# Kernel optimization log

Measured on AMD Instinct MI355X. Metric: run time of the kernel, lower is better.

## Reference

```python
import jax, jax.numpy as jnp
import numpy as np

UNITS = 256

def setup_inputs() -> dict:
    key = jax.random.key(0)
    k1, k2, k3, k4 = jax.random.split(key, 4)
    B, T, F = 131072, 7, 60
    x = jax.random.normal(k1, (B, T, F), dtype=jnp.float32)
    W = jax.random.normal(k2, (F, 4 * UNITS), dtype=jnp.float32) * 0.05
    U = jax.random.normal(k3, (UNITS, 4 * UNITS), dtype=jnp.float32) * 0.05
    b = jax.random.normal(k4, (4 * UNITS,), dtype=jnp.float32) * 0.05
    return {"x": x, "W": W, "U": U, "b": b}

def reference(x, W, U, b):
    # Keras LSTM, return_sequences=False, return_state=True -> (last_h, h, c).
    # Gate order in the fused kernel: i, f, c(g), o. Inference path (no dropout).
    B = x.shape[0]
    h0 = jnp.zeros((B, UNITS), dtype=x.dtype)
    c0 = jnp.zeros((B, UNITS), dtype=x.dtype)

    def step(carry, xt):
        h, c = carry
        z = xt @ W + h @ U + b  # [B, 4*UNITS]
        zi, zf, zg, zo = jnp.split(z, 4, axis=-1)
        i = jax.nn.sigmoid(zi)
        f = jax.nn.sigmoid(zf)
        g = jnp.tanh(zg)
        o = jax.nn.sigmoid(zo)
        c_new = f * c + i * g
        h_new = o * jnp.tanh(c_new)
        return (h_new, c_new), None

    xs = jnp.transpose(x, (1, 0, 2))  # [T, B, F]
    (h, c), _ = jax.lax.scan(step, (h0, c0), xs)
    return h, h, c
```

## Files before the change

### kernel.cpp

```cpp
#include <hip/hip_runtime.h>

typedef __bf16 bf16x8 __attribute__((ext_vector_type(8)));
typedef float f32x4 __attribute__((ext_vector_type(4)));

#define TSTEPS 7
#define FEAT 60
#define MTILE 64
#define THREADS 256

__global__ void prep_U_kernel(const float* __restrict__ U, __bf16* __restrict__ Ut) {
    int idx = blockIdx.x * blockDim.x + threadIdx.x;
    int n = idx >> 8;
    int k = idx & 255;
    Ut[idx] = (__bf16)U[k * 1024 + n];
}

__global__ void prep_W_kernel(const float* __restrict__ W, __bf16* __restrict__ Wt) {
    int idx = blockIdx.x * blockDim.x + threadIdx.x;
    int n = idx >> 6;
    int k = idx & 63;
    float v = (k < FEAT) ? W[k * 1024 + n] : 0.0f;
    Wt[idx] = (__bf16)v;
}

__device__ __forceinline__ float sigm(float z) {
    return __builtin_amdgcn_rcpf(1.0f + __expf(-z));
}
__device__ __forceinline__ float tanh_(float z) {
    return 1.0f - 2.0f * __builtin_amdgcn_rcpf(__expf(2.0f * z) + 1.0f);
}

__global__ __launch_bounds__(THREADS, 2)
void lstm_kernel(const float* __restrict__ x, const __bf16* __restrict__ Ut,
                 const __bf16* __restrict__ Wt, const float* __restrict__ bias,
                 float* __restrict__ out, int B) {
    __shared__ __align__(16) __bf16 x_lds[2][MTILE][72];
    __shared__ __align__(16) __bf16 h_lds[MTILE][264];

    const int tid = threadIdx.x;
    const int wave = tid >> 6;
    const int lane = tid & 63;
    const int quad = lane >> 4;
    const int l16 = lane & 15;
    const int r0 = blockIdx.x * MTILE;

    for (int i = tid; i < 2 * MTILE * 4; i += THREADS) {
        int bb = i >> 8;
        int rem = i & 255;
        x_lds[bb][rem >> 2][FEAT + (rem & 3)] = (__bf16)0.0f;
    }

    auto stage_x = [&](int t, int b) {
        for (int i = tid; i < MTILE * 15; i += THREADS) {
            int m = i / 15;
            int q = i - m * 15;
            const float4 v =
                *(const float4*)&x[((size_t)(r0 + m) * TSTEPS + t) * FEAT + q * 4];
            __bf16* dst = &x_lds[b][m][q * 4];
            dst[0] = (__bf16)v.x;
            dst[1] = (__bf16)v.y;
            dst[2] = (__bf16)v.z;
            dst[3] = (__bf16)v.w;
        }
    };

    stage_x(0, 0);

    float c_reg[4][4][4];
#pragma unroll
    for (int uc = 0; uc < 4; ++uc)
#pragma unroll
        for (int mt = 0; mt < 4; ++mt)
#pragma unroll
            for (int r = 0; r < 4; ++r) c_reg[uc][mt][r] = 0.0f;

    float bvals[4][4];
#pragma unroll
    for (int uc = 0; uc < 4; ++uc)
#pragma unroll
        for (int g = 0; g < 4; ++g)
            bvals[uc][g] = bias[g * 256 + wave * 64 + uc * 16 + l16];

    __syncthreads();

    const size_t HN = (size_t)B * 256;

    for (int t = 0; t < TSTEPS; ++t) {
        const int xb = t & 1;
        bf16x8 a[4][10];
        if (t > 0) {
#pragma unroll
            for (int mt = 0; mt < 4; ++mt)
#pragma unroll
                for (int kf = 0; kf < 8; ++kf)
                    a[mt][kf] = *(const bf16x8*)&h_lds[mt * 16 + l16][kf * 32 + quad * 8];
        }
#pragma unroll
        for (int mt = 0; mt < 4; ++mt) {
            a[mt][8] = *(const bf16x8*)&x_lds[xb][mt * 16 + l16][quad * 8];
            a[mt][9] = *(const bf16x8*)&x_lds[xb][mt * 16 + l16][32 + quad * 8];
        }
        __syncthreads();

        if (t + 1 < TSTEPS) stage_x(t + 1, xb ^ 1);

#pragma unroll
        for (int uc = 0; uc < 4; ++uc) {
            const int ncol = wave * 64 + uc * 16 + l16;
            f32x4 acc[4];

            auto gate_gemm = [&](int g) {
                const __bf16* uRow = Ut + (size_t)(g * 256 + ncol) * 256;
                const __bf16* wRow = Wt + (size_t)(g * 256 + ncol) * 64;
                bf16x8 bfr[10];
                if (t > 0) {
#pragma unroll
                    for (int kf = 0; kf < 8; ++kf)
                        bfr[kf] = *(const bf16x8*)(uRow + kf * 32 + quad * 8);
                }
#pragma unroll
                for (int kf = 0; kf < 2; ++kf)
                    bfr[8 + kf] = *(const bf16x8*)(wRow + kf * 32 + quad * 8);
#pragma unroll
                for (int mt = 0; mt < 4; ++mt) acc[mt] = (f32x4){0.f, 0.f, 0.f, 0.f};
                if (t > 0) {
#pragma unroll
                    for (int kf = 0; kf < 8; ++kf)
#pragma unroll
                        for (int mt = 0; mt < 4; ++mt)
                            acc[mt] = __builtin_amdgcn_mfma_f32_16x16x32_bf16(
                                a[mt][kf], bfr[kf], acc[mt], 0, 0, 0);
                }
#pragma unroll
                for (int kf = 0; kf < 2; ++kf)
#pragma unroll
                    for (int mt = 0; mt < 4; ++mt)
                        acc[mt] = __builtin_amdgcn_mfma_f32_16x16x32_bf16(
                            a[mt][8 + kf], bfr[8 + kf], acc[mt], 0, 0, 0);
            };

            float iv[4][4], pg[4][4];
            gate_gemm(0);
#pragma unroll
            for (int mt = 0; mt < 4; ++mt)
#pragma unroll
                for (int r = 0; r < 4; ++r)
                    iv[mt][r] = sigm(acc[mt][r] + bvals[uc][0]);
            gate_gemm(2);
#pragma unroll
            for (int mt = 0; mt < 4; ++mt)
#pragma unroll
                for (int r = 0; r < 4; ++r)
                    pg[mt][r] = iv[mt][r] * tanh_(acc[mt][r] + bvals[uc][2]);
            gate_gemm(1);
#pragma unroll
            for (int mt = 0; mt < 4; ++mt)
#pragma unroll
                for (int r = 0; r < 4; ++r)
                    c_reg[uc][mt][r] =
                        sigm(acc[mt][r] + bvals[uc][1]) * c_reg[uc][mt][r] + pg[mt][r];
            gate_gemm(3);
#pragma unroll
            for (int mt = 0; mt < 4; ++mt)
#pragma unroll
                for (int r = 0; r < 4; ++r) {
                    float cc = c_reg[uc][mt][r];
                    float hv = sigm(acc[mt][r] + bvals[uc][3]) * tanh_(cc);
                    h_lds[mt * 16 + quad * 4 + r][ncol] = (__bf16)hv;
                    if (t == TSTEPS - 1) {
                        size_t mg = (size_t)(r0 + mt * 16 + quad * 4 + r);
                        out[mg * 256 + ncol] = hv;
                        out[HN + mg * 256 + ncol] = hv;
                        out[2 * HN + mg * 256 + ncol] = cc;
                    }
                }
        }
        __syncthreads();
    }
}

extern "C" void kernel_launch(void* const* d_in, const int* in_sizes, int n_in,
                              void* d_out, int out_size, void* d_ws, size_t ws_size,
                              hipStream_t stream) {
    const float* x = (const float*)d_in[0];
    const float* W = (const float*)d_in[1];
    const float* U = (const float*)d_in[2];
    const float* b = (const float*)d_in[3];
    float* out = (float*)d_out;

    const int B = in_sizes[0] / (TSTEPS * FEAT);

    __bf16* Ut = (__bf16*)d_ws;
    __bf16* Wt = (__bf16*)((char*)d_ws + 1024 * 256 * 2);

    prep_U_kernel<<<1024, 256, 0, stream>>>(U, Ut);
    prep_W_kernel<<<256, 256, 0, stream>>>(W, Wt);
    lstm_kernel<<<B / MTILE, THREADS, 0, stream>>>(x, Ut, Wt, b, out, B);
}
```

Measured before the change: 2.849 ms.

## Enlarge LSTM block tile to 128 rows and fuse all four gate GEMMs

Doubles the batch tile per block to 128 rows with 8 waves (2 row groups by 4 column groups), so each U/W fragment loaded from global memory feeds twice as many rows. The four gate GEMMs are interleaved in one k-loop so each A fragment read from LDS is shared across all gates, and the bias is folded into the accumulator initialisation. The next timestep's x is prefetched into registers and h is double-buffered in LDS. The cost is much higher register pressure (16 accumulators plus c state), with the minimum-occupancy hint dropped, which risks spills or lower occupancy.

```diff
diff --git a/kernel.cpp b/kernel.cpp
--- a/kernel.cpp
+++ b/kernel.cpp
@@ -5,8 +5,9 @@
 
 #define TSTEPS 7
 #define FEAT 60
-#define MTILE 64
-#define THREADS 256
+#define MTILE 128
+#define THREADS 512
+#define XCHUNKS (MTILE * 15)
 
 __global__ void prep_U_kernel(const float* __restrict__ U, __bf16* __restrict__ Ut) {
     int idx = blockIdx.x * blockDim.x + threadIdx.x;
@@ -30,42 +31,35 @@
     return 1.0f - 2.0f * __builtin_amdgcn_rcpf(__expf(2.0f * z) + 1.0f);
 }
 
-__global__ __launch_bounds__(THREADS, 2)
+__global__ __launch_bounds__(THREADS)
 void lstm_kernel(const float* __restrict__ x, const __bf16* __restrict__ Ut,
                  const __bf16* __restrict__ Wt, const float* __restrict__ bias,
                  float* __restrict__ out, int B) {
-    __shared__ __align__(16) __bf16 x_lds[2][MTILE][72];
-    __shared__ __align__(16) __bf16 h_lds[MTILE][264];
+    __shared__ __align__(16) __bf16 h_lds[2][MTILE][264];
+    __shared__ __align__(16) __bf16 x_lds[MTILE][72];
 
     const int tid = threadIdx.x;
     const int wave = tid >> 6;
     const int lane = tid & 63;
     const int quad = lane >> 4;
     const int l16 = lane & 15;
+    const int wrow = (wave >> 2) * 64;
+    const int wcol = (wave & 3) * 64;
     const int r0 = blockIdx.x * MTILE;
 
-    for (int i = tid; i < 2 * MTILE * 4; i += THREADS) {
-        int bb = i >> 8;
-        int rem = i & 255;
-        x_lds[bb][rem >> 2][FEAT + (rem & 3)] = (__bf16)0.0f;
+    x_lds[tid >> 2][FEAT + (tid & 3)] = (__bf16)0.0f;
+
+    for (int i = tid; i < XCHUNKS; i += THREADS) {
+        int m = i / 15;
+        int q = i - m * 15;
+        const float4 v = *(const float4*)&x[(size_t)(r0 + m) * (TSTEPS * FEAT) + q * 4];
+        __bf16* dst = &x_lds[m][q * 4];
+        dst[0] = (__bf16)v.x;
+        dst[1] = (__bf16)v.y;
+        dst[2] = (__bf16)v.z;
+        dst[3] = (__bf16)v.w;
     }
 
-    auto stage_x = [&](int t, int b) {
-        for (int i = tid; i < MTILE * 15; i += THREADS) {
-            int m = i / 15;
-            int q = i - m * 15;
-            const float4 v =
-                *(const float4*)&x[((size_t)(r0 + m) * TSTEPS + t) * FEAT + q * 4];
-            __bf16* dst = &x_lds[b][m][q * 4];
-            dst[0] = (__bf16)v.x;
-            dst[1] = (__bf16)v.y;
-            dst[2] = (__bf16)v.z;
-            dst[3] = (__bf16)v.w;
-        }
-    };
-
-    stage_x(0, 0);
-
     float c_reg[4][4][4];
 #pragma unroll
     for (int uc = 0; uc < 4; ++uc)
@@ -79,103 +73,126 @@
     for (int uc = 0; uc < 4; ++uc)
 #pragma unroll
         for (int g = 0; g < 4; ++g)
-            bvals[uc][g] = bias[g * 256 + wave * 64 + uc * 16 + l16];
+            bvals[uc][g] = bias[g * 256 + wcol + uc * 16 + l16];
 
     __syncthreads();
 
     const size_t HN = (size_t)B * 256;
 
+#pragma unroll 1
     for (int t = 0; t < TSTEPS; ++t) {
-        const int xb = t & 1;
-        bf16x8 a[4][10];
-        if (t > 0) {
-#pragma unroll
-            for (int mt = 0; mt < 4; ++mt)
-#pragma unroll
-                for (int kf = 0; kf < 8; ++kf)
-                    a[mt][kf] = *(const bf16x8*)&h_lds[mt * 16 + l16][kf * 32 + quad * 8];
-        }
+        const int rb = t & 1;
+        const int wb = rb ^ 1;
+
+        float4 xr[4];
+        if (t + 1 < TSTEPS) {
+#pragma unroll
+            for (int k = 0; k < 4; ++k) {
+                int i = tid + k * THREADS;
+                if (i < XCHUNKS) {
+                    int m = i / 15;
+                    int q = i - m * 15;
+                    xr[k] = *(const float4*)&x[((size_t)(r0 + m) * TSTEPS + (t + 1)) * FEAT + q * 4];
+                }
+            }
+        }
+
+        bf16x8 ax[4][2];
 #pragma unroll
         for (int mt = 0; mt < 4; ++mt) {
-            a[mt][8] = *(const bf16x8*)&x_lds[xb][mt * 16 + l16][quad * 8];
-            a[mt][9] = *(const bf16x8*)&x_lds[xb][mt * 16 + l16][32 + quad * 8];
-        }
-        __syncthreads();
-
-        if (t + 1 < TSTEPS) stage_x(t + 1, xb ^ 1);
+#pragma unroll
+            for (int kx = 0; kx < 2; ++kx)
+                ax[mt][kx] = *(const bf16x8*)&x_lds[wrow + mt * 16 + l16][kx * 32 + quad * 8];
+        }
 
 #pragma unroll
         for (int uc = 0; uc < 4; ++uc) {
-            const int ncol = wave * 64 + uc * 16 + l16;
-            f32x4 acc[4];
-
-            auto gate_gemm = [&](int g) {
-                const __bf16* uRow = Ut + (size_t)(g * 256 + ncol) * 256;
-                const __bf16* wRow = Wt + (size_t)(g * 256 + ncol) * 64;
-                bf16x8 bfr[10];
-                if (t > 0) {
-#pragma unroll
-                    for (int kf = 0; kf < 8; ++kf)
-                        bfr[kf] = *(const bf16x8*)(uRow + kf * 32 + quad * 8);
-                }
-#pragma unroll
-                for (int kf = 0; kf < 2; ++kf)
-                    bfr[8 + kf] = *(const bf16x8*)(wRow + kf * 32 + quad * 8);
-#pragma unroll
-                for (int mt = 0; mt < 4; ++mt) acc[mt] = (f32x4){0.f, 0.f, 0.f, 0.f};
-                if (t > 0) {
-#pragma unroll
-                    for (int kf = 0; kf < 8; ++kf)
-#pragma unroll
-                        for (int mt = 0; mt < 4; ++mt)
-                            acc[mt] = __builtin_amdgcn_mfma_f32_16x16x32_bf16(
-                                a[mt][kf], bfr[kf], acc[mt], 0, 0, 0);
-                }
-#pragma unroll
-                for (int kf = 0; kf < 2; ++kf)
-#pragma unroll
-                    for (int mt = 0; mt < 4; ++mt)
-                        acc[mt] = __builtin_amdgcn_mfma_f32_16x16x32_bf16(
-                            a[mt][8 + kf], bfr[8 + kf], acc[mt], 0, 0, 0);
-            };
-
-            float iv[4][4], pg[4][4];
-            gate_gemm(0);
-#pragma unroll
-            for (int mt = 0; mt < 4; ++mt)
-#pragma unroll
-                for (int r = 0; r < 4; ++r)
-                    iv[mt][r] = sigm(acc[mt][r] + bvals[uc][0]);
-            gate_gemm(2);
-#pragma unroll
-            for (int mt = 0; mt < 4; ++mt)
-#pragma unroll
-                for (int r = 0; r < 4; ++r)
-                    pg[mt][r] = iv[mt][r] * tanh_(acc[mt][r] + bvals[uc][2]);
-            gate_gemm(1);
-#pragma unroll
-            for (int mt = 0; mt < 4; ++mt)
-#pragma unroll
-                for (int r = 0; r < 4; ++r)
-                    c_reg[uc][mt][r] =
-                        sigm(acc[mt][r] + bvals[uc][1]) * c_reg[uc][mt][r] + pg[mt][r];
-            gate_gemm(3);
-#pragma unroll
-            for (int mt = 0; mt < 4; ++mt)
+            const int ncol = wcol + uc * 16 + l16;
+            const __bf16* uBase = Ut + (size_t)ncol * 256;
+            const __bf16* wBase = Wt + (size_t)ncol * 64;
+
+            f32x4 acc[4][4];
+#pragma unroll
+            for (int g = 0; g < 4; ++g) {
+                const float bv = bvals[uc][g];
+#pragma unroll
+                for (int mt = 0; mt < 4; ++mt) acc[g][mt] = (f32x4){bv, bv, bv, bv};
+            }
+
+            if (t > 0) {
+#pragma unroll
+                for (int kf = 0; kf < 8; ++kf) {
+                    const int ko = kf * 32 + quad * 8;
+                    bf16x8 b0 = *(const bf16x8*)(uBase + 0 * 65536 + ko);
+                    bf16x8 b1 = *(const bf16x8*)(uBase + 1 * 65536 + ko);
+                    bf16x8 b2 = *(const bf16x8*)(uBase + 2 * 65536 + ko);
+                    bf16x8 b3 = *(const bf16x8*)(uBase + 3 * 65536 + ko);
+#pragma unroll
+                    for (int mt = 0; mt < 4; ++mt) {
+                        bf16x8 a = *(const bf16x8*)&h_lds[rb][wrow + mt * 16 + l16][ko];
+                        acc[0][mt] = __builtin_amdgcn_mfma_f32_16x16x32_bf16(a, b0, acc[0][mt], 0, 0, 0);
+                        acc[1][mt] = __builtin_amdgcn_mfma_f32_16x16x32_bf16(a, b1, acc[1][mt], 0, 0, 0);
+                        acc[2][mt] = __builtin_amdgcn_mfma_f32_16x16x32_bf16(a, b2, acc[2][mt], 0, 0, 0);
+                        acc[3][mt] = __builtin_amdgcn_mfma_f32_16x16x32_bf16(a, b3, acc[3][mt], 0, 0, 0);
+                    }
+                }
+            }
+#pragma unroll
+            for (int kx = 0; kx < 2; ++kx) {
+                const int ko = kx * 32 + quad * 8;
+                bf16x8 b0 = *(const bf16x8*)(wBase + 0 * 16384 + ko);
+                bf16x8 b1 = *(const bf16x8*)(wBase + 1 * 16384 + ko);
+                bf16x8 b2 = *(const bf16x8*)(wBase + 2 * 16384 + ko);
+                bf16x8 b3 = *(const bf16x8*)(wBase + 3 * 16384 + ko);
+#pragma unroll
+                for (int mt = 0; mt < 4; ++mt) {
+                    acc[0][mt] = __builtin_amdgcn_mfma_f32_16x16x32_bf16(ax[mt][kx], b0, acc[0][mt], 0, 0, 0);
+                    acc[1][mt] = __builtin_amdgcn_mfma_f32_16x16x32_bf16(ax[mt][kx], b1, acc[1][mt], 0, 0, 0);
+                    acc[2][mt] = __builtin_amdgcn_mfma_f32_16x16x32_bf16(ax[mt][kx], b2, acc[2][mt], 0, 0, 0);
+                    acc[3][mt] = __builtin_amdgcn_mfma_f32_16x16x32_bf16(ax[mt][kx], b3, acc[3][mt], 0, 0, 0);
+                }
+            }
+
+#pragma unroll
+            for (int mt = 0; mt < 4; ++mt) {
 #pragma unroll
                 for (int r = 0; r < 4; ++r) {
-                    float cc = c_reg[uc][mt][r];
-                    float hv = sigm(acc[mt][r] + bvals[uc][3]) * tanh_(cc);
-                    h_lds[mt * 16 + quad * 4 + r][ncol] = (__bf16)hv;
+                    float iv = sigm(acc[0][mt][r]);
+                    float fv = sigm(acc[1][mt][r]);
+                    float gv = tanh_(acc[2][mt][r]);
+                    float ov = sigm(acc[3][mt][r]);
+                    float cc = fv * c_reg[uc][mt][r] + iv * gv;
+                    c_reg[uc][mt][r] = cc;
+                    float hv = ov * tanh_(cc);
+                    const int row = wrow + mt * 16 + quad * 4 + r;
+                    h_lds[wb][row][ncol] = (__bf16)hv;
                     if (t == TSTEPS - 1) {
-                        size_t mg = (size_t)(r0 + mt * 16 + quad * 4 + r);
+                        size_t mg = (size_t)(r0 + row);
                         out[mg * 256 + ncol] = hv;
                         out[HN + mg * 256 + ncol] = hv;
                         out[2 * HN + mg * 256 + ncol] = cc;
                     }
                 }
-        }
-        __syncthreads();
+            }
+        }
+
+        if (t + 1 < TSTEPS) {
+            __syncthreads();
+#pragma unroll
+            for (int k = 0; k < 4; ++k) {
+                int i = tid + k * THREADS;
+                if (i < XCHUNKS) {
+                    int m = i / 15;
+                    int q = i - m * 15;
+                    __bf16* dst = &x_lds[m][q * 4];
+                    dst[0] = (__bf16)xr[k].x;
+                    dst[1] = (__bf16)xr[k].y;
+                    dst[2] = (__bf16)xr[k].z;
+                    dst[3] = (__bf16)xr[k].w;
+                }
+            }
+            __syncthreads();
+        }
     }
 }
 
```

Result: slower. 4.014 ms (+40.9%).
